# Optimization experiments

Measured on AMD Instinct MI355X. Metric: run time of the kernel, lower is better.

## Reference

```python
import jax, jax.numpy as jnp
import numpy as np

S, B, I = 512, 64, 1024
H = 1024 // 2  # per-direction hidden (MyBiGRU halves hidden_size)


def _gru(x, h0, Wx, Wh, b):
    """Single-direction GRU, faithful to MyGRU.forward.
    x: (S,B,I); h0: (B,H); Wx: (3,I,H) gates [r,u,h]; Wh: (3,H,H); b: (3,H).
    Note: candidate uses (reset_gate * state) @ Whh, matching torch operator
    precedence in `reset_gate * state @ self.weight_hh`.
    """
    # Precompute all input projections once: (S, 3, B, H)
    xg = jnp.einsum('sbi,gih->sgbh', x, Wx)

    def step(h, xt):
        r = jax.nn.sigmoid(xt[0] + h @ Wh[0] + b[0])
        u = jax.nn.sigmoid(xt[1] + h @ Wh[1] + b[1])
        c = jnp.tanh(xt[2] + (r * h) @ Wh[2] + b[2])
        h_new = u * h + (1.0 - u) * c
        return h_new, h_new

    h_last, hs = jax.lax.scan(step, h0, xg)
    return hs, h_last  # (S,B,H), (B,H)


def setup_inputs() -> dict:
    key = jax.random.key(0)
    ks = jax.random.split(key, 6)
    std = jnp.float32(0.01)
    return {
        "x": jax.random.normal(ks[0], (S, B, I), jnp.float32),
        "initial_state": jax.random.normal(ks[1], (B, 2 * H), jnp.float32),
        "Wx_f": std * jax.random.normal(ks[2], (3, I, H), jnp.float32),
        "Wh_f": std * jax.random.normal(ks[3], (3, H, H), jnp.float32),
        "b_f": jnp.zeros((3, H), jnp.float32),
        "Wx_b": std * jax.random.normal(ks[4], (3, I, H), jnp.float32),
        "Wh_b": std * jax.random.normal(ks[5], (3, H, H), jnp.float32),
        "b_b": jnp.zeros((3, H), jnp.float32),
    }


def reference(x, initial_state, Wx_f, Wh_f, b_f, Wx_b, Wh_b, b_b):
    h0_f = initial_state[:, :H]
    h0_b = initial_state[:, H:]
    fwd_out, fwd_state = _gru(x, h0_f, Wx_f, Wh_f, b_f)
    bwd_out, bwd_state = _gru(x[::-1], h0_b, Wx_b, Wh_b, b_b)
    outputs = jnp.concatenate([fwd_out, bwd_out[::-1]], axis=-1)  # (S,B,2H)
    state = jnp.concatenate([fwd_state, bwd_state], axis=-1)      # (B,2H)
    return outputs, state
```

## Files before the change

kernel.cpp:

```cpp
#include <hip/hip_runtime.h>
#include <hip/hip_bf16.h>


typedef __attribute__((ext_vector_type(8))) short short8;
typedef __attribute__((ext_vector_type(4))) float f32x4;

#define SENT 0x7FC0
#define SENT64 0x7FC07FC07FC07FC0ULL

__device__ __forceinline__ unsigned short f2bf(float f) {
    unsigned u = __builtin_bit_cast(unsigned, f);
    u += 0x7FFFu + ((u >> 16) & 1u);
    return (unsigned short)(u >> 16);
}
__device__ __forceinline__ float bf2f(unsigned short h) {
    unsigned u = ((unsigned)h) << 16;
    return __builtin_bit_cast(float, u);
}
__device__ __forceinline__ float xv(unsigned long long p, int jj) {
    return bf2f((unsigned short)(p >> (16 * jj)));
}
__device__ __forceinline__ int imin(int a, int b) { return a < b ? a : b; }


__global__ __launch_bounds__(256) void k_cvt_x(const float* __restrict__ x,
                                               unsigned short* __restrict__ xb) {
    size_t gid = (size_t)blockIdx.x * 256 + threadIdx.x;
    f32x4 a = ((const f32x4*)x)[gid * 2];
    f32x4 b = ((const f32x4*)x)[gid * 2 + 1];
    short8 o;
    o[0] = (short)f2bf(a[0]); o[1] = (short)f2bf(a[1]);
    o[2] = (short)f2bf(a[2]); o[3] = (short)f2bf(a[3]);
    o[4] = (short)f2bf(b[0]); o[5] = (short)f2bf(b[1]);
    o[6] = (short)f2bf(b[2]); o[7] = (short)f2bf(b[3]);
    ((short8*)xb)[gid] = o;
}

__global__ __launch_bounds__(256) void k_cvt_w(const float* __restrict__ Wxf,
                                               const float* __restrict__ Wxb,
                                               unsigned short* __restrict__ wt) {
    int gid = blockIdx.x * 256 + threadIdx.x;
    int n = gid >> 7, kc = gid & 127;
    const float* src = (n < 1536) ? Wxf : Wxb;
    int nn = (n >= 1536) ? n - 1536 : n;
    int g = nn >> 9, h = nn & 511;
    short8 o;
#pragma unroll
    for (int j = 0; j < 8; ++j)
        o[j] = (short)f2bf(src[(size_t)(g * 1024 + kc * 8 + j) * 512 + h]);
    *(short8*)(wt + (size_t)n * 1024 + kc * 8) = o;
}

__global__ __launch_bounds__(256) void k_cvt_whsl(const float* __restrict__ Whf,
                                                  const float* __restrict__ Whb,
                                                  unsigned short* __restrict__ o) {
    int gid = blockIdx.x * 256 + threadIdx.x;
    int kc = gid & 63;
    int r = gid >> 6;
    int c = r & 15; r >>= 4;
    int g = r % 3;  r /= 3;
    int w = r & 31, d = r >> 5;
    const float* src = d ? Whb : Whf;
    short8 v;
#pragma unroll
    for (int j = 0; j < 8; ++j)
        v[j] = (short)f2bf(src[(size_t)(g * 512 + kc * 8 + j) * 512 + w * 16 + c]);
    *(short8*)(o + ((size_t)((d * 32 + w) * 3 + g) * 16 + c) * 512 + kc * 8) = v;
}

__global__ __launch_bounds__(256) void k_sent(unsigned short* __restrict__ h4,
                                              unsigned short* __restrict__ rh4) {
    int gid = blockIdx.x * 256 + threadIdx.x;
    short8 s;
#pragma unroll
    for (int j = 0; j < 8; ++j) s[j] = (short)SENT;
    ((short8*)h4)[gid] = s;
    ((short8*)rh4)[gid] = s;
}

__global__ __launch_bounds__(256) void k_init(const float* __restrict__ h0,
                                              unsigned short* __restrict__ h4) {
    int gid = blockIdx.x * 256 + threadIdx.x;
    int b = gid >> 10, ch = gid & 1023;
    int d = ch >> 9, k = ch & 511;
    h4[((size_t)d * 64 + b) * 512 + k] = f2bf(h0[gid]);
}


__global__ __launch_bounds__(256) void k_gemm(const unsigned short* __restrict__ A,
                                              const unsigned short* __restrict__ Bt,
                                              unsigned short* __restrict__ C) {
    __shared__ unsigned short Al[128 * 40];
    __shared__ unsigned short Bl[128 * 40];
    const int n0 = blockIdx.x * 128;
    const int m0 = blockIdx.y * 128;
    const int t = threadIdx.x, wave = t >> 6, lane = t & 63;
    const int lg = lane >> 4, lr = lane & 15;
    const int wm = wave >> 1, wn = wave & 1;
    const int lrow = t >> 2, lkb = t & 3;

    f32x4 acc[4][4] = {};
    for (int kt = 0; kt < 32; ++kt) {
        const int k0 = kt * 32;
#pragma unroll
        for (int p = 0; p < 2; ++p) {
            int row = lrow + p * 64;
            *(short8*)(Al + row * 40 + lkb * 8) =
                *(const short8*)(A + (size_t)(m0 + row) * 1024 + k0 + lkb * 8);
            *(short8*)(Bl + row * 40 + lkb * 8) =
                *(const short8*)(Bt + (size_t)(n0 + row) * 1024 + k0 + lkb * 8);
        }
        __syncthreads();
        short8 af[4], bfr[4];
#pragma unroll
        for (int mi = 0; mi < 4; ++mi)
            af[mi] = *(const short8*)(Al + (wm * 64 + mi * 16 + lr) * 40 + lg * 8);
#pragma unroll
        for (int ni = 0; ni < 4; ++ni)
            bfr[ni] = *(const short8*)(Bl + (wn * 64 + ni * 16 + lr) * 40 + lg * 8);
#pragma unroll
        for (int mi = 0; mi < 4; ++mi)
#pragma unroll
            for (int ni = 0; ni < 4; ++ni)
                acc[mi][ni] = __builtin_amdgcn_mfma_f32_16x16x32_bf16(af[mi], bfr[ni],
                                                                      acc[mi][ni], 0, 0, 0);
        __syncthreads();
    }
#pragma unroll
    for (int mi = 0; mi < 4; ++mi)
#pragma unroll
        for (int ni = 0; ni < 4; ++ni) {
            int m = m0 + wm * 64 + mi * 16 + lg * 4;
            int n = n0 + wn * 64 + ni * 16 + lr;
            int dd = n >= 1536;
            int nn = n - dd * 1536;
            int g = nn >> 9, h = nn & 511;
            size_t colbase = (size_t)dd * 98304 + (size_t)(h >> 4) * 3072 +
                             (size_t)((h >> 2) & 3) * 12 + g * 4 + (h & 3);
#pragma unroll
            for (int jj = 0; jj < 4; ++jj) {
                int mm = m + jj;
                int s = mm >> 6, brow = mm & 63;
                C[(size_t)s * 196608 + colbase + (size_t)brow * 48] = f2bf(acc[mi][ni][jj]);
            }
        }
}


__device__ __forceinline__ void wait_frag(const char* p, short8* fr) {
    for (;;) {
        asm volatile(
            "global_load_dwordx4 %0, %16, off sc1\n\t"
            "global_load_dwordx4 %1, %16, off offset:64 sc1\n\t"
            "global_load_dwordx4 %2, %16, off offset:128 sc1\n\t"
            "global_load_dwordx4 %3, %16, off offset:192 sc1\n\t"
            "global_load_dwordx4 %4, %16, off offset:256 sc1\n\t"
            "global_load_dwordx4 %5, %16, off offset:320 sc1\n\t"
            "global_load_dwordx4 %6, %16, off offset:384 sc1\n\t"
            "global_load_dwordx4 %7, %16, off offset:448 sc1\n\t"
            "global_load_dwordx4 %8, %16, off offset:512 sc1\n\t"
            "global_load_dwordx4 %9, %16, off offset:576 sc1\n\t"
            "global_load_dwordx4 %10, %16, off offset:640 sc1\n\t"
            "global_load_dwordx4 %11, %16, off offset:704 sc1\n\t"
            "global_load_dwordx4 %12, %16, off offset:768 sc1\n\t"
            "global_load_dwordx4 %13, %16, off offset:832 sc1\n\t"
            "global_load_dwordx4 %14, %16, off offset:896 sc1\n\t"
            "global_load_dwordx4 %15, %16, off offset:960 sc1"
            : "=v"(fr[0]), "=v"(fr[1]), "=v"(fr[2]), "=v"(fr[3]),
              "=v"(fr[4]), "=v"(fr[5]), "=v"(fr[6]), "=v"(fr[7]),
              "=v"(fr[8]), "=v"(fr[9]), "=v"(fr[10]), "=v"(fr[11]),
              "=v"(fr[12]), "=v"(fr[13]), "=v"(fr[14]), "=v"(fr[15])
            : "v"(p) : "memory");
        asm volatile("s_waitcnt vmcnt(0)" ::: "memory");
        int bad = 0;
#pragma unroll
        for (int i = 0; i < 16; ++i)
            bad |= (((unsigned short)fr[i][0]) == SENT) |
                   (((unsigned short)fr[i][4]) == SENT);
        if (!__any(bad)) break;
        __builtin_amdgcn_s_sleep(2);
    }
    __builtin_amdgcn_sched_barrier(0);
}


__global__ __launch_bounds__(320) void k_rec(const unsigned short* __restrict__ xgr,
                                             const unsigned short* __restrict__ whsl,
                                             const float* __restrict__ h0,
                                             const float* __restrict__ b_f,
                                             const float* __restrict__ b_b,
                                             unsigned long long* h4,
                                             unsigned long long* rh4,
                                             float* __restrict__ out) {
    __shared__ char Wlb[98304];
    __shared__ char xls[24576];
    __shared__ int xg_ready;
    __shared__ int xg_ack[4];

    const int w = blockIdx.x;
    const int t = threadIdx.x;
    const int wave5 = t >> 6, lane = t & 63;

    if (t == 0) {
        xg_ready = 0;
        xg_ack[0] = xg_ack[1] = xg_ack[2] = xg_ack[3] = 0;
    }
    for (int i = 0; i < 20; ++i) {
        int c = t + i * 320;
        if (c < 6144) {
            int half = (c >= 3072);
            int byte = (c - half * 3072) << 4;
            int swz = byte ^ (((byte >> 10) & 7) << 4);
            *(short8*)(Wlb + half * 49152 + swz) =
                *(const short8*)((const char*)whsl + (size_t)(half * 32 + w) * 49152 + byte);
        }
    }
    __syncthreads();

    if (wave5 == 4) {
        for (int it = 0; it < 512; ++it) {
            if (it >= 2) {
                for (;;) {
                    int a0 = __hip_atomic_load(&xg_ack[0], __ATOMIC_RELAXED, __HIP_MEMORY_SCOPE_WORKGROUP);
                    int a1 = __hip_atomic_load(&xg_ack[1], __ATOMIC_RELAXED, __HIP_MEMORY_SCOPE_WORKGROUP);
                    int a2 = __hip_atomic_load(&xg_ack[2], __ATOMIC_RELAXED, __HIP_MEMORY_SCOPE_WORKGROUP);
                    int a3 = __hip_atomic_load(&xg_ack[3], __ATOMIC_RELAXED, __HIP_MEMORY_SCOPE_WORKGROUP);
                    if (imin(imin(a0, a1), imin(a2, a3)) >= it - 1) break;
                    __builtin_amdgcn_s_sleep(1);
                }
            }
            const char* pf = (const char*)xgr + (size_t)it * 393216 +
                             (size_t)w * 6144 + lane * 96;
            const char* pb = (const char*)xgr + (size_t)(511 - it) * 393216 + 196608 +
                             (size_t)w * 6144 + lane * 96;
            short8 vf[6], vb[6];
#pragma unroll
            for (int k = 0; k < 6; ++k) {
                vf[k] = *(const short8*)(pf + k * 16);
                vb[k] = *(const short8*)(pb + k * 16);
            }
            char* dst = xls + (it & 1) * 12288 + lane * 96;
#pragma unroll
            for (int k = 0; k < 6; ++k) {
                *(short8*)(dst + k * 16) = vf[k];
                *(short8*)(dst + 6144 + k * 16) = vb[k];
            }
            __builtin_amdgcn_fence(__ATOMIC_RELEASE, "workgroup");
            if (lane == 0)
                __hip_atomic_store(&xg_ready, it + 1, __ATOMIC_RELAXED, __HIP_MEMORY_SCOPE_WORKGROUP);
        }
        return;
    }

    const int wave = wave5, lg = lane >> 4, lr = lane & 15;
    const int b = wave * 16 + lr;
    const int cc = w * 16 + lg * 4;
    const int cswz = (lr & 7) << 4;

    const f32x4 bRf = *(const f32x4*)(b_f + cc);
    const f32x4 bUf = *(const f32x4*)(b_f + 512 + cc);
    const f32x4 bCf = *(const f32x4*)(b_f + 1024 + cc);
    const f32x4 bRb = *(const f32x4*)(b_b + cc);
    const f32x4 bUb = *(const f32x4*)(b_b + 512 + cc);
    const f32x4 bCb = *(const f32x4*)(b_b + 1024 + cc);

    float hf[4], hbo[4];
#pragma unroll
    for (int jj = 0; jj < 4; ++jj) {
        hf[jj]  = h0[(size_t)b * 1024 + cc + jj];
        hbo[jj] = h0[(size_t)b * 1024 + 512 + cc + jj];
    }

    const size_t rof = (size_t)b * 1024;
    const size_t rob = (size_t)(64 + b) * 1024;
    const int fro  = lg * 16;
    const int pubo = w * 32 + lg * 8;
    const int xoff = (b * 4 + lg) * 24;
    char* hbP = (char*)h4;
    char* rbP = (char*)rh4;

    for (int it = 0; it < 512; ++it) {
        const size_t slot  = (size_t)(it & 3) << 17;
        const size_t nslot = (size_t)((it + 1) & 3) << 17;
        const size_t oslot = (size_t)((it + 3) & 3) << 17;

        short8 fr[16];
        wait_frag(hbP + slot + rof + fro, fr);
        __hip_atomic_store((unsigned long long*)(hbP + oslot + rof + pubo), SENT64,
                           __ATOMIC_RELAXED, __HIP_MEMORY_SCOPE_AGENT);

        while (__hip_atomic_load(&xg_ready, __ATOMIC_RELAXED, __HIP_MEMORY_SCOPE_WORKGROUP) < it + 1)
            __builtin_amdgcn_s_sleep(1);
        __builtin_amdgcn_fence(__ATOMIC_ACQUIRE, "workgroup");
        const char* xp = xls + (it & 1) * 12288 + xoff;
        const unsigned long long xfR = *(const unsigned long long*)(xp);
        const unsigned long long xfU = *(const unsigned long long*)(xp + 8);
        const unsigned long long xfC = *(const unsigned long long*)(xp + 16);
        const unsigned long long xbR = *(const unsigned long long*)(xp + 6144);
        const unsigned long long xbU = *(const unsigned long long*)(xp + 6144 + 8);
        const unsigned long long xbC = *(const unsigned long long*)(xp + 6144 + 16);

        f32x4 aR = {0.f, 0.f, 0.f, 0.f}, aU = {0.f, 0.f, 0.f, 0.f};
#pragma unroll
        for (int ks = 0; ks < 16; ++ks) {
            int koff = ks * 64 + lg * 16;
            short8 w0 = *(const short8*)(Wlb + (((lr << 10) + koff) ^ cswz));
            short8 w1 = *(const short8*)(Wlb + ((16384 + (lr << 10) + koff) ^ cswz));
            aR = __builtin_amdgcn_mfma_f32_16x16x32_bf16(w0, fr[ks], aR, 0, 0, 0);
            aU = __builtin_amdgcn_mfma_f32_16x16x32_bf16(w1, fr[ks], aU, 0, 0, 0);
        }
        float uf[4];
        {
            unsigned long long rhp = 0;
#pragma unroll
            for (int jj = 0; jj < 4; ++jj) {
                float pr = aR[jj] + xv(xfR, jj) + bRf[jj];
                float pu = aU[jj] + xv(xfU, jj) + bUf[jj];
                float r = 1.f / (1.f + __expf(-pr));
                uf[jj] = 1.f / (1.f + __expf(-pu));
                rhp |= (unsigned long long)f2bf(r * hf[jj]) << (16 * jj);
            }
            __hip_atomic_store((unsigned long long*)(rbP + slot + rof + pubo), rhp,
                               __ATOMIC_RELAXED, __HIP_MEMORY_SCOPE_AGENT);
        }

        short8 fb[16];
        wait_frag(hbP + slot + rob + fro, fb);
        __hip_atomic_store((unsigned long long*)(hbP + oslot + rob + pubo), SENT64,
                           __ATOMIC_RELAXED, __HIP_MEMORY_SCOPE_AGENT);

        f32x4 cR = {0.f, 0.f, 0.f, 0.f}, cU = {0.f, 0.f, 0.f, 0.f};
#pragma unroll
        for (int ks = 0; ks < 16; ++ks) {
            int koff = ks * 64 + lg * 16;
            short8 w0 = *(const short8*)(Wlb + 49152 + (((lr << 10) + koff) ^ cswz));
            short8 w1 = *(const short8*)(Wlb + 49152 + ((16384 + (lr << 10) + koff) ^ cswz));
            cR = __builtin_amdgcn_mfma_f32_16x16x32_bf16(w0, fb[ks], cR, 0, 0, 0);
            cU = __builtin_amdgcn_mfma_f32_16x16x32_bf16(w1, fb[ks], cU, 0, 0, 0);
        }
        float ub[4];
        {
            unsigned long long rhp = 0;
#pragma unroll
            for (int jj = 0; jj < 4; ++jj) {
                float pr = cR[jj] + xv(xbR, jj) + bRb[jj];
                float pu = cU[jj] + xv(xbU, jj) + bUb[jj];
                float r = 1.f / (1.f + __expf(-pr));
                ub[jj] = 1.f / (1.f + __expf(-pu));
                rhp |= (unsigned long long)f2bf(r * hbo[jj]) << (16 * jj);
            }
            __hip_atomic_store((unsigned long long*)(rbP + slot + rob + pubo), rhp,
                               __ATOMIC_RELAXED, __HIP_MEMORY_SCOPE_AGENT);
        }

        short8 gr[16];
        wait_frag(rbP + slot + rof + fro, gr);
        __hip_atomic_store((unsigned long long*)(rbP + oslot + rof + pubo), SENT64,
                           __ATOMIC_RELAXED, __HIP_MEMORY_SCOPE_AGENT);

        f32x4 aC = {0.f, 0.f, 0.f, 0.f};
#pragma unroll
        for (int ks = 0; ks < 16; ++ks) {
            int koff = ks * 64 + lg * 16;
            short8 w2 = *(const short8*)(Wlb + ((32768 + (lr << 10) + koff) ^ cswz));
            aC = __builtin_amdgcn_mfma_f32_16x16x32_bf16(w2, gr[ks], aC, 0, 0, 0);
        }
        {
            f32x4 ov;
            unsigned long long hp = 0;
#pragma unroll
            for (int jj = 0; jj < 4; ++jj) {
                float pc = aC[jj] + xv(xfC, jj) + bCf[jj];
                float e = __expf(-2.f * pc);
                float c = 2.f / (1.f + e) - 1.f;
                float hn = uf[jj] * hf[jj] + (1.f - uf[jj]) * c;
                hf[jj] = hn;
                ov[jj] = hn;
                hp |= (unsigned long long)f2bf(hn) << (16 * jj);
            }
            __hip_atomic_store((unsigned long long*)(hbP + nslot + rof + pubo), hp,
                               __ATOMIC_RELAXED, __HIP_MEMORY_SCOPE_AGENT);
            *(f32x4*)(out + ((size_t)it * 64 + b) * 1024 + cc) = ov;
        }

        short8 gb[16];
        wait_frag(rbP + slot + rob + fro, gb);
        __hip_atomic_store((unsigned long long*)(rbP + oslot + rob + pubo), SENT64,
                           __ATOMIC_RELAXED, __HIP_MEMORY_SCOPE_AGENT);

        f32x4 cC = {0.f, 0.f, 0.f, 0.f};
#pragma unroll
        for (int ks = 0; ks < 16; ++ks) {
            int koff = ks * 64 + lg * 16;
            short8 w2 = *(const short8*)(Wlb + 49152 + ((32768 + (lr << 10) + koff) ^ cswz));
            cC = __builtin_amdgcn_mfma_f32_16x16x32_bf16(w2, gb[ks], cC, 0, 0, 0);
        }
        {
            f32x4 ov;
            unsigned long long hp = 0;
#pragma unroll
            for (int jj = 0; jj < 4; ++jj) {
                float pc = cC[jj] + xv(xbC, jj) + bCb[jj];
                float e = __expf(-2.f * pc);
                float c = 2.f / (1.f + e) - 1.f;
                float hn = ub[jj] * hbo[jj] + (1.f - ub[jj]) * c;
                hbo[jj] = hn;
                ov[jj] = hn;
                hp |= (unsigned long long)f2bf(hn) << (16 * jj);
            }
            __hip_atomic_store((unsigned long long*)(hbP + nslot + rob + pubo), hp,
                               __ATOMIC_RELAXED, __HIP_MEMORY_SCOPE_AGENT);
            *(f32x4*)(out + ((size_t)(511 - it) * 64 + b) * 1024 + 512 + cc) = ov;
        }

        if (lane == 0)
            __hip_atomic_store(&xg_ack[wave], it + 1, __ATOMIC_RELAXED, __HIP_MEMORY_SCOPE_WORKGROUP);
    }

    {
        f32x4 of = {hf[0], hf[1], hf[2], hf[3]};
        f32x4 ob = {hbo[0], hbo[1], hbo[2], hbo[3]};
        *(f32x4*)(out + (size_t)33554432 + (size_t)b * 1024 + cc) = of;
        *(f32x4*)(out + (size_t)33554432 + (size_t)b * 1024 + 512 + cc) = ob;
    }
}


extern "C" void kernel_launch(void* const* d_in, const int* in_sizes, int n_in,
                              void* d_out, int out_size, void* d_ws, size_t ws_size,
                              hipStream_t stream) {
    const float* x   = (const float*)d_in[0];
    const float* h0  = (const float*)d_in[1];
    const float* Wxf = (const float*)d_in[2];
    const float* Whf = (const float*)d_in[3];
    const float* bf_ = (const float*)d_in[4];
    const float* Wxb = (const float*)d_in[5];
    const float* Whb = (const float*)d_in[6];
    const float* bb_ = (const float*)d_in[7];
    float* out = (float*)d_out;

    char* ws = (char*)d_ws;
    size_t off = 0;
    auto take = [&](size_t bytes) {
        char* p = ws + off;
        off += (bytes + 255) & ~(size_t)255;
        return p;
    };
    unsigned short* xb   = (unsigned short*)take((size_t)33554432 * 2);
    unsigned short* wt   = (unsigned short*)take((size_t)3072 * 1024 * 2);
    unsigned short* xgr  = (unsigned short*)take((size_t)512 * 196608 * 2);
    unsigned short* whsl = (unsigned short*)take((size_t)2 * 32 * 3 * 16 * 512 * 2);
    unsigned long long* h4  = (unsigned long long*)take((size_t)4 * 131072);
    unsigned long long* rh4 = (unsigned long long*)take((size_t)4 * 131072);

    if (off > ws_size) return;

    hipLaunchKernelGGL(k_cvt_x,    dim3(16384),   dim3(256), 0, stream, x, xb);
    hipLaunchKernelGGL(k_cvt_w,    dim3(1536),    dim3(256), 0, stream, Wxf, Wxb, wt);
    hipLaunchKernelGGL(k_cvt_whsl, dim3(768),     dim3(256), 0, stream, Whf, Whb, whsl);
    hipLaunchKernelGGL(k_sent,     dim3(128),     dim3(256), 0, stream,
                       (unsigned short*)h4, (unsigned short*)rh4);
    hipLaunchKernelGGL(k_init,     dim3(256),     dim3(256), 0, stream, h0,
                       (unsigned short*)h4);
    hipLaunchKernelGGL(k_gemm,     dim3(24, 256), dim3(256), 0, stream, xb, wt, xgr);
    hipLaunchKernelGGL(k_rec,      dim3(32),      dim3(320), 0, stream, xgr, whsl, h0,
                       bf_, bb_, h4, rh4, out);
}
```

Before: 4.901 ms.

## Split forward and backward directions across separate waves in recurrent kernel

```diff
diff --git a/kernel.cpp b/kernel.cpp
--- a/kernel.cpp
+++ b/kernel.cpp
@@ -20,7 +20,6 @@
 __device__ __forceinline__ float xv(unsigned long long p, int jj) {
     return bf2f((unsigned short)(p >> (16 * jj)));
 }
-__device__ __forceinline__ int imin(int a, int b) { return a < b ? a : b; }
 
 
 __global__ __launch_bounds__(256) void k_cvt_x(const float* __restrict__ x,
@@ -178,35 +177,33 @@
             bad |= (((unsigned short)fr[i][0]) == SENT) |
                    (((unsigned short)fr[i][4]) == SENT);
         if (!__any(bad)) break;
-        __builtin_amdgcn_s_sleep(2);
+        __builtin_amdgcn_s_sleep(1);
     }
     __builtin_amdgcn_sched_barrier(0);
 }
 
 
-__global__ __launch_bounds__(320) void k_rec(const unsigned short* __restrict__ xgr,
-                                             const unsigned short* __restrict__ whsl,
-                                             const float* __restrict__ h0,
-                                             const float* __restrict__ b_f,
-                                             const float* __restrict__ b_b,
-                                             unsigned long long* h4,
-                                             unsigned long long* rh4,
-                                             float* __restrict__ out) {
+__global__ __launch_bounds__(576, 1) void k_rec(const unsigned short* __restrict__ xgr,
+                                                const unsigned short* __restrict__ whsl,
+                                                const float* __restrict__ h0,
+                                                const float* __restrict__ b_f,
+                                                const float* __restrict__ b_b,
+                                                unsigned long long* h4,
+                                                unsigned long long* rh4,
+                                                float* __restrict__ out) {
     __shared__ char Wlb[98304];
     __shared__ char xls[24576];
     __shared__ int xg_ready;
-    __shared__ int xg_ack[4];
+    __shared__ int xg_ack[8];
 
     const int w = blockIdx.x;
     const int t = threadIdx.x;
-    const int wave5 = t >> 6, lane = t & 63;
-
-    if (t == 0) {
-        xg_ready = 0;
-        xg_ack[0] = xg_ack[1] = xg_ack[2] = xg_ack[3] = 0;
-    }
-    for (int i = 0; i < 20; ++i) {
-        int c = t + i * 320;
+    const int wv = t >> 6, lane = t & 63;
+
+    if (t == 0) xg_ready = 0;
+    if (t < 8) xg_ack[t] = 0;
+    for (int i = 0; i < 11; ++i) {
+        int c = t + i * 576;
         if (c < 6144) {
             int half = (c >= 3072);
             int byte = (c - half * 3072) << 4;
@@ -217,15 +214,18 @@
     }
     __syncthreads();
 
-    if (wave5 == 4) {
+    if (wv == 8) {
         for (int it = 0; it < 512; ++it) {
             if (it >= 2) {
                 for (;;) {
-                    int a0 = __hip_atomic_load(&xg_ack[0], __ATOMIC_RELAXED, __HIP_MEMORY_SCOPE_WORKGROUP);
-                    int a1 = __hip_atomic_load(&xg_ack[1], __ATOMIC_RELAXED, __HIP_MEMORY_SCOPE_WORKGROUP);
-                    int a2 = __hip_atomic_load(&xg_ack[2], __ATOMIC_RELAXED, __HIP_MEMORY_SCOPE_WORKGROUP);
-                    int a3 = __hip_atomic_load(&xg_ack[3], __ATOMIC_RELAXED, __HIP_MEMORY_SCOPE_WORKGROUP);
-                    if (imin(imin(a0, a1), imin(a2, a3)) >= it - 1) break;
+                    int mn = 0x7FFFFFFF;
+#pragma unroll
+                    for (int q = 0; q < 8; ++q) {
+                        int a = __hip_atomic_load(&xg_ack[q], __ATOMIC_RELAXED,
+                                                  __HIP_MEMORY_SCOPE_WORKGROUP);
+                        mn = a < mn ? a : mn;
+                    }
+                    if (mn >= it - 1) break;
                     __builtin_amdgcn_s_sleep(1);
                 }
             }
@@ -247,122 +247,89 @@
             }
             __builtin_amdgcn_fence(__ATOMIC_RELEASE, "workgroup");
             if (lane == 0)
-                __hip_atomic_store(&xg_ready, it + 1, __ATOMIC_RELAXED, __HIP_MEMORY_SCOPE_WORKGROUP);
+                __hip_atomic_store(&xg_ready, it + 1, __ATOMIC_RELAXED,
+                                   __HIP_MEMORY_SCOPE_WORKGROUP);
         }
         return;
     }
 
-    const int wave = wave5, lg = lane >> 4, lr = lane & 15;
-    const int b = wave * 16 + lr;
+    const int dir = wv >> 2;
+    const int lg = lane >> 4, lr = lane & 15;
+    const int b = (wv & 3) * 16 + lr;
     const int cc = w * 16 + lg * 4;
     const int cswz = (lr & 7) << 4;
-
-    const f32x4 bRf = *(const f32x4*)(b_f + cc);
-    const f32x4 bUf = *(const f32x4*)(b_f + 512 + cc);
-    const f32x4 bCf = *(const f32x4*)(b_f + 1024 + cc);
-    const f32x4 bRb = *(const f32x4*)(b_b + cc);
-    const f32x4 bUb = *(const f32x4*)(b_b + 512 + cc);
-    const f32x4 bCb = *(const f32x4*)(b_b + 1024 + cc);
-
-    float hf[4], hbo[4];
-#pragma unroll
-    for (int jj = 0; jj < 4; ++jj) {
-        hf[jj]  = h0[(size_t)b * 1024 + cc + jj];
-        hbo[jj] = h0[(size_t)b * 1024 + 512 + cc + jj];
-    }
-
-    const size_t rof = (size_t)b * 1024;
-    const size_t rob = (size_t)(64 + b) * 1024;
+    const char* Wd = Wlb + dir * 49152;
+    const float* bias = dir ? b_b : b_f;
+
+    const f32x4 bR = *(const f32x4*)(bias + cc);
+    const f32x4 bU = *(const f32x4*)(bias + 512 + cc);
+    const f32x4 bC = *(const f32x4*)(bias + 1024 + cc);
+
+    float hst[4];
+#pragma unroll
+    for (int jj = 0; jj < 4; ++jj)
+        hst[jj] = h0[(size_t)b * 1024 + dir * 512 + cc + jj];
+
+    const size_t row = (size_t)(dir * 64 + b) * 1024;
     const int fro  = lg * 16;
     const int pubo = w * 32 + lg * 8;
-    const int xoff = (b * 4 + lg) * 24;
     char* hbP = (char*)h4;
     char* rbP = (char*)rh4;
 
     for (int it = 0; it < 512; ++it) {
+        const int s = dir ? (511 - it) : it;
         const size_t slot  = (size_t)(it & 3) << 17;
         const size_t nslot = (size_t)((it + 1) & 3) << 17;
         const size_t oslot = (size_t)((it + 3) & 3) << 17;
 
         short8 fr[16];
-        wait_frag(hbP + slot + rof + fro, fr);
-        __hip_atomic_store((unsigned long long*)(hbP + oslot + rof + pubo), SENT64,
+        wait_frag(hbP + slot + row + fro, fr);
+        __hip_atomic_store((unsigned long long*)(hbP + oslot + row + pubo), SENT64,
                            __ATOMIC_RELAXED, __HIP_MEMORY_SCOPE_AGENT);
 
-        while (__hip_atomic_load(&xg_ready, __ATOMIC_RELAXED, __HIP_MEMORY_SCOPE_WORKGROUP) < it + 1)
+        while (__hip_atomic_load(&xg_ready, __ATOMIC_RELAXED,
+                                 __HIP_MEMORY_SCOPE_WORKGROUP) < it + 1)
             __builtin_amdgcn_s_sleep(1);
         __builtin_amdgcn_fence(__ATOMIC_ACQUIRE, "workgroup");
-        const char* xp = xls + (it & 1) * 12288 + xoff;
-        const unsigned long long xfR = *(const unsigned long long*)(xp);
-        const unsigned long long xfU = *(const unsigned long long*)(xp + 8);
-        const unsigned long long xfC = *(const unsigned long long*)(xp + 16);
-        const unsigned long long xbR = *(const unsigned long long*)(xp + 6144);
-        const unsigned long long xbU = *(const unsigned long long*)(xp + 6144 + 8);
-        const unsigned long long xbC = *(const unsigned long long*)(xp + 6144 + 16);
+        const char* xp = xls + (it & 1) * 12288 + dir * 6144 + (b * 4 + lg) * 24;
+        const unsigned long long xR = *(const unsigned long long*)(xp);
+        const unsigned long long xU = *(const unsigned long long*)(xp + 8);
+        const unsigned long long xC = *(const unsigned long long*)(xp + 16);
 
         f32x4 aR = {0.f, 0.f, 0.f, 0.f}, aU = {0.f, 0.f, 0.f, 0.f};
 #pragma unroll
         for (int ks = 0; ks < 16; ++ks) {
             int koff = ks * 64 + lg * 16;
-            short8 w0 = *(const short8*)(Wlb + (((lr << 10) + koff) ^ cswz));
-            short8 w1 = *(const short8*)(Wlb + ((16384 + (lr << 10) + koff) ^ cswz));
+            short8 w0 = *(const short8*)(Wd + (((lr << 10) + koff) ^ cswz));
+            short8 w1 = *(const short8*)(Wd + ((16384 + (lr << 10) + koff) ^ cswz));
             aR = __builtin_amdgcn_mfma_f32_16x16x32_bf16(w0, fr[ks], aR, 0, 0, 0);
             aU = __builtin_amdgcn_mfma_f32_16x16x32_bf16(w1, fr[ks], aU, 0, 0, 0);
         }
-        float uf[4];
+        float uu[4];
         {
             unsigned long long rhp = 0;
 #pragma unroll
             for (int jj = 0; jj < 4; ++jj) {
-                float pr = aR[jj] + xv(xfR, jj) + bRf[jj];
-                float pu = aU[jj] + xv(xfU, jj) + bUf[jj];
+                float pr = aR[jj] + xv(xR, jj) + bR[jj];
+                float pu = aU[jj] + xv(xU, jj) + bU[jj];
                 float r = 1.f / (1.f + __expf(-pr));
-                uf[jj] = 1.f / (1.f + __expf(-pu));
-                rhp |= (unsigned long long)f2bf(r * hf[jj]) << (16 * jj);
-            }
-            __hip_atomic_store((unsigned long long*)(rbP + slot + rof + pubo), rhp,
+                uu[jj] = 1.f / (1.f + __expf(-pu));
+                rhp |= (unsigned long long)f2bf(r * hst[jj]) << (16 * jj);
+            }
+            __hip_atomic_store((unsigned long long*)(rbP + slot + row + pubo), rhp,
                                __ATOMIC_RELAXED, __HIP_MEMORY_SCOPE_AGENT);
         }
 
-        short8 fb[16];
-        wait_frag(hbP + slot + rob + fro, fb);
-        __hip_atomic_store((unsigned long long*)(hbP + oslot + rob + pubo), SENT64,
+        short8 gr[16];
+        wait_frag(rbP + slot + row + fro, gr);
+        __hip_atomic_store((unsigned long long*)(rbP + oslot + row + pubo), SENT64,
                            __ATOMIC_RELAXED, __HIP_MEMORY_SCOPE_AGENT);
 
-        f32x4 cR = {0.f, 0.f, 0.f, 0.f}, cU = {0.f, 0.f, 0.f, 0.f};
+        f32x4 aC = {0.f, 0.f, 0.f, 0.f};
 #pragma unroll
         for (int ks = 0; ks < 16; ++ks) {
             int koff = ks * 64 + lg * 16;
-            short8 w0 = *(const short8*)(Wlb + 49152 + (((lr << 10) + koff) ^ cswz));
-            short8 w1 = *(const short8*)(Wlb + 49152 + ((16384 + (lr << 10) + koff) ^ cswz));
-            cR = __builtin_amdgcn_mfma_f32_16x16x32_bf16(w0, fb[ks], cR, 0, 0, 0);
-            cU = __builtin_amdgcn_mfma_f32_16x16x32_bf16(w1, fb[ks], cU, 0, 0, 0);
-        }
-        float ub[4];
-        {
-            unsigned long long rhp = 0;
-#pragma unroll
-            for (int jj = 0; jj < 4; ++jj) {
-                float pr = cR[jj] + xv(xbR, jj) + bRb[jj];
-                float pu = cU[jj] + xv(xbU, jj) + bUb[jj];
-                float r = 1.f / (1.f + __expf(-pr));
-                ub[jj] = 1.f / (1.f + __expf(-pu));
-                rhp |= (unsigned long long)f2bf(r * hbo[jj]) << (16 * jj);
-            }
-            __hip_atomic_store((unsigned long long*)(rbP + slot + rob + pubo), rhp,
-                               __ATOMIC_RELAXED, __HIP_MEMORY_SCOPE_AGENT);
-        }
-
-        short8 gr[16];
-        wait_frag(rbP + slot + rof + fro, gr);
-        __hip_atomic_store((unsigned long long*)(rbP + oslot + rof + pubo), SENT64,
-                           __ATOMIC_RELAXED, __HIP_MEMORY_SCOPE_AGENT);
-
-        f32x4 aC = {0.f, 0.f, 0.f, 0.f};
-#pragma unroll
-        for (int ks = 0; ks < 16; ++ks) {
-            int koff = ks * 64 + lg * 16;
-            short8 w2 = *(const short8*)(Wlb + ((32768 + (lr << 10) + koff) ^ cswz));
+            short8 w2 = *(const short8*)(Wd + ((32768 + (lr << 10) + koff) ^ cswz));
             aC = __builtin_amdgcn_mfma_f32_16x16x32_bf16(w2, gr[ks], aC, 0, 0, 0);
         }
         {
@@ -370,58 +337,27 @@
             unsigned long long hp = 0;
 #pragma unroll
             for (int jj = 0; jj < 4; ++jj) {
-                float pc = aC[jj] + xv(xfC, jj) + bCf[jj];
+                float pc = aC[jj] + xv(xC, jj) + bC[jj];
                 float e = __expf(-2.f * pc);
                 float c = 2.f / (1.f + e) - 1.f;
-                float hn = uf[jj] * hf[jj] + (1.f - uf[jj]) * c;
-                hf[jj] = hn;
+                float hn = uu[jj] * hst[jj] + (1.f - uu[jj]) * c;
+                hst[jj] = hn;
                 ov[jj] = hn;
                 hp |= (unsigned long long)f2bf(hn) << (16 * jj);
             }
-            __hip_atomic_store((unsigned long long*)(hbP + nslot + rof + pubo), hp,
+            __hip_atomic_store((unsigned long long*)(hbP + nslot + row + pubo), hp,
                                __ATOMIC_RELAXED, __HIP_MEMORY_SCOPE_AGENT);
-            *(f32x4*)(out + ((size_t)it * 64 + b) * 1024 + cc) = ov;
-        }
-
-        short8 gb[16];
-        wait_frag(rbP + slot + rob + fro, gb);
-        __hip_atomic_store((unsigned long long*)(rbP + oslot + rob + pubo), SENT64,
-                           __ATOMIC_RELAXED, __HIP_MEMORY_SCOPE_AGENT);
-
-        f32x4 cC = {0.f, 0.f, 0.f, 0.f};
-#pragma unroll
-        for (int ks = 0; ks < 16; ++ks) {
-            int koff = ks * 64 + lg * 16;
-            short8 w2 = *(const short8*)(Wlb + 49152 + ((32768 + (lr << 10) + koff) ^ cswz));
-            cC = __builtin_amdgcn_mfma_f32_16x16x32_bf16(w2, gb[ks], cC, 0, 0, 0);
-        }
-        {
-            f32x4 ov;
-            unsigned long long hp = 0;
-#pragma unroll
-            for (int jj = 0; jj < 4; ++jj) {
-                float pc = cC[jj] + xv(xbC, jj) + bCb[jj];
-                float e = __expf(-2.f * pc);
-                float c = 2.f / (1.f + e) - 1.f;
-                float hn = ub[jj] * hbo[jj] + (1.f - ub[jj]) * c;
-                hbo[jj] = hn;
-                ov[jj] = hn;
-                hp |= (unsigned long long)f2bf(hn) << (16 * jj);
-            }
-            __hip_atomic_store((unsigned long long*)(hbP + nslot + rob + pubo), hp,
-                               __ATOMIC_RELAXED, __HIP_MEMORY_SCOPE_AGENT);
-            *(f32x4*)(out + ((size_t)(511 - it) * 64 + b) * 1024 + 512 + cc) = ov;
+            *(f32x4*)(out + ((size_t)s * 64 + b) * 1024 + dir * 512 + cc) = ov;
         }
 
         if (lane == 0)
-            __hip_atomic_store(&xg_ack[wave], it + 1, __ATOMIC_RELAXED, __HIP_MEMORY_SCOPE_WORKGROUP);
+            __hip_atomic_store(&xg_ack[wv], it + 1, __ATOMIC_RELAXED,
+                               __HIP_MEMORY_SCOPE_WORKGROUP);
     }
 
     {
-        f32x4 of = {hf[0], hf[1], hf[2], hf[3]};
-        f32x4 ob = {hbo[0], hbo[1], hbo[2], hbo[3]};
-        *(f32x4*)(out + (size_t)33554432 + (size_t)b * 1024 + cc) = of;
-        *(f32x4*)(out + (size_t)33554432 + (size_t)b * 1024 + 512 + cc) = ob;
+        f32x4 of = {hst[0], hst[1], hst[2], hst[3]};
+        *(f32x4*)(out + (size_t)33554432 + (size_t)b * 1024 + dir * 512 + cc) = of;
     }
 }
 
@@ -463,6 +399,6 @@
     hipLaunchKernelGGL(k_init,     dim3(256),     dim3(256), 0, stream, h0,
                        (unsigned short*)h4);
     hipLaunchKernelGGL(k_gemm,     dim3(24, 256), dim3(256), 0, stream, xb, wt, xgr);
-    hipLaunchKernelGGL(k_rec,      dim3(32),      dim3(320), 0, stream, xgr, whsl, h0,
+    hipLaunchKernelGGL(k_rec,      dim3(32),      dim3(576), 0, stream, xgr, whsl, h0,
                        bf_, bb_, h4, rh4, out);
 }
```

After: 9.092 ms. +85.5%, slower.

## Prefetch next recurrent fragments speculatively with partial vmcnt waits

Applied to the files above, without the earlier changes.

```diff
diff --git a/kernel.cpp b/kernel.cpp
--- a/kernel.cpp
+++ b/kernel.cpp
@@ -147,39 +147,59 @@
 }
 
 
+__device__ __forceinline__ void load16(const char* p, short8* fr) {
+    asm volatile(
+        "global_load_dwordx4 %0, %16, off sc1\n\t"
+        "global_load_dwordx4 %1, %16, off offset:64 sc1\n\t"
+        "global_load_dwordx4 %2, %16, off offset:128 sc1\n\t"
+        "global_load_dwordx4 %3, %16, off offset:192 sc1\n\t"
+        "global_load_dwordx4 %4, %16, off offset:256 sc1\n\t"
+        "global_load_dwordx4 %5, %16, off offset:320 sc1\n\t"
+        "global_load_dwordx4 %6, %16, off offset:384 sc1\n\t"
+        "global_load_dwordx4 %7, %16, off offset:448 sc1\n\t"
+        "global_load_dwordx4 %8, %16, off offset:512 sc1\n\t"
+        "global_load_dwordx4 %9, %16, off offset:576 sc1\n\t"
+        "global_load_dwordx4 %10, %16, off offset:640 sc1\n\t"
+        "global_load_dwordx4 %11, %16, off offset:704 sc1\n\t"
+        "global_load_dwordx4 %12, %16, off offset:768 sc1\n\t"
+        "global_load_dwordx4 %13, %16, off offset:832 sc1\n\t"
+        "global_load_dwordx4 %14, %16, off offset:896 sc1\n\t"
+        "global_load_dwordx4 %15, %16, off offset:960 sc1"
+        : "=v"(fr[0]), "=v"(fr[1]), "=v"(fr[2]), "=v"(fr[3]),
+          "=v"(fr[4]), "=v"(fr[5]), "=v"(fr[6]), "=v"(fr[7]),
+          "=v"(fr[8]), "=v"(fr[9]), "=v"(fr[10]), "=v"(fr[11]),
+          "=v"(fr[12]), "=v"(fr[13]), "=v"(fr[14]), "=v"(fr[15])
+        : "v"(p) : "memory");
+}
+
+__device__ __forceinline__ int chk(const short8* fr) {
+    int bad = 0;
+#pragma unroll
+    for (int i = 0; i < 16; ++i)
+        bad |= (((unsigned short)fr[i][0]) == SENT) |
+               (((unsigned short)fr[i][4]) == SENT);
+    return __any(bad);
+}
+
 __device__ __forceinline__ void wait_frag(const char* p, short8* fr) {
     for (;;) {
-        asm volatile(
-            "global_load_dwordx4 %0, %16, off sc1\n\t"
-            "global_load_dwordx4 %1, %16, off offset:64 sc1\n\t"
-            "global_load_dwordx4 %2, %16, off offset:128 sc1\n\t"
-            "global_load_dwordx4 %3, %16, off offset:192 sc1\n\t"
-            "global_load_dwordx4 %4, %16, off offset:256 sc1\n\t"
-            "global_load_dwordx4 %5, %16, off offset:320 sc1\n\t"
-            "global_load_dwordx4 %6, %16, off offset:384 sc1\n\t"
-            "global_load_dwordx4 %7, %16, off offset:448 sc1\n\t"
-            "global_load_dwordx4 %8, %16, off offset:512 sc1\n\t"
-            "global_load_dwordx4 %9, %16, off offset:576 sc1\n\t"
-            "global_load_dwordx4 %10, %16, off offset:640 sc1\n\t"
-            "global_load_dwordx4 %11, %16, off offset:704 sc1\n\t"
-            "global_load_dwordx4 %12, %16, off offset:768 sc1\n\t"
-            "global_load_dwordx4 %13, %16, off offset:832 sc1\n\t"
-            "global_load_dwordx4 %14, %16, off offset:896 sc1\n\t"
-            "global_load_dwordx4 %15, %16, off offset:960 sc1"
-            : "=v"(fr[0]), "=v"(fr[1]), "=v"(fr[2]), "=v"(fr[3]),
-              "=v"(fr[4]), "=v"(fr[5]), "=v"(fr[6]), "=v"(fr[7]),
-              "=v"(fr[8]), "=v"(fr[9]), "=v"(fr[10]), "=v"(fr[11]),
-              "=v"(fr[12]), "=v"(fr[13]), "=v"(fr[14]), "=v"(fr[15])
-            : "v"(p) : "memory");
+        load16(p, fr);
         asm volatile("s_waitcnt vmcnt(0)" ::: "memory");
-        int bad = 0;
-#pragma unroll
-        for (int i = 0; i < 16; ++i)
-            bad |= (((unsigned short)fr[i][0]) == SENT) |
-                   (((unsigned short)fr[i][4]) == SENT);
-        if (!__any(bad)) break;
+        __builtin_amdgcn_sched_barrier(0);
+        if (!chk(fr)) break;
         __builtin_amdgcn_s_sleep(2);
     }
+}
+
+template<int N> __device__ __forceinline__ void wait_vm() {
+    asm volatile("s_waitcnt vmcnt(%0)" :: "i"(N) : "memory");
+}
+
+template<int N>
+__device__ __forceinline__ void check_or_wait(const char* p, short8* fr) {
+    wait_vm<N>();
+    __builtin_amdgcn_sched_barrier(0);
+    if (chk(fr)) wait_frag(p, fr);
     __builtin_amdgcn_sched_barrier(0);
 }
 
@@ -279,13 +299,17 @@
     char* hbP = (char*)h4;
     char* rbP = (char*)rh4;
 
+    short8 fr0[16], fr1[16];
+    load16(hbP + rof + fro, fr0);
+    load16(hbP + rob + fro, fr1);
+
     for (int it = 0; it < 512; ++it) {
         const size_t slot  = (size_t)(it & 3) << 17;
         const size_t nslot = (size_t)((it + 1) & 3) << 17;
         const size_t oslot = (size_t)((it + 3) & 3) << 17;
 
-        short8 fr[16];
-        wait_frag(hbP + slot + rof + fro, fr);
+        if (it == 0) check_or_wait<16>(hbP + slot + rof + fro, fr0);
+        else         check_or_wait<20>(hbP + slot + rof + fro, fr0);
         __hip_atomic_store((unsigned long long*)(hbP + oslot + rof + pubo), SENT64,
                            __ATOMIC_RELAXED, __HIP_MEMORY_SCOPE_AGENT);
 
@@ -306,8 +330,8 @@
             int koff = ks * 64 + lg * 16;
             short8 w0 = *(const short8*)(Wlb + (((lr << 10) + koff) ^ cswz));
             short8 w1 = *(const short8*)(Wlb + ((16384 + (lr << 10) + koff) ^ cswz));
-            aR = __builtin_amdgcn_mfma_f32_16x16x32_bf16(w0, fr[ks], aR, 0, 0, 0);
-            aU = __builtin_amdgcn_mfma_f32_16x16x32_bf16(w1, fr[ks], aU, 0, 0, 0);
+            aR = __builtin_amdgcn_mfma_f32_16x16x32_bf16(w0, fr0[ks], aR, 0, 0, 0);
+            aU = __builtin_amdgcn_mfma_f32_16x16x32_bf16(w1, fr0[ks], aU, 0, 0, 0);
         }
         float uf[4];
         {
@@ -323,9 +347,10 @@
             __hip_atomic_store((unsigned long long*)(rbP + slot + rof + pubo), rhp,
                                __ATOMIC_RELAXED, __HIP_MEMORY_SCOPE_AGENT);
         }
-
-        short8 fb[16];
-        wait_frag(hbP + slot + rob + fro, fb);
+        __builtin_amdgcn_sched_barrier(0);
+        load16(rbP + slot + rof + fro, fr0);
+
+        check_or_wait<18>(hbP + slot + rob + fro, fr1);
         __hip_atomic_store((unsigned long long*)(hbP + oslot + rob + pubo), SENT64,
                            __ATOMIC_RELAXED, __HIP_MEMORY_SCOPE_AGENT);
 
@@ -335,8 +360,8 @@
             int koff = ks * 64 + lg * 16;
             short8 w0 = *(const short8*)(Wlb + 49152 + (((lr << 10) + koff) ^ cswz));
             short8 w1 = *(const short8*)(Wlb + 49152 + ((16384 + (lr << 10) + koff) ^ cswz));
-            cR = __builtin_amdgcn_mfma_f32_16x16x32_bf16(w0, fb[ks], cR, 0, 0, 0);
-            cU = __builtin_amdgcn_mfma_f32_16x16x32_bf16(w1, fb[ks], cU, 0, 0, 0);
+            cR = __builtin_amdgcn_mfma_f32_16x16x32_bf16(w0, fr1[ks], cR, 0, 0, 0);
+            cU = __builtin_amdgcn_mfma_f32_16x16x32_bf16(w1, fr1[ks], cU, 0, 0, 0);
         }
         float ub[4];
         {
@@ -352,9 +377,10 @@
             __hip_atomic_store((unsigned long long*)(rbP + slot + rob + pubo), rhp,
                                __ATOMIC_RELAXED, __HIP_MEMORY_SCOPE_AGENT);
         }
-
-        short8 gr[16];
-        wait_frag(rbP + slot + rof + fro, gr);
+        __builtin_amdgcn_sched_barrier(0);
+        load16(rbP + slot + rob + fro, fr1);
+
+        check_or_wait<18>(rbP + slot + rof + fro, fr0);
         __hip_atomic_store((unsigned long long*)(rbP + oslot + rof + pubo), SENT64,
                            __ATOMIC_RELAXED, __HIP_MEMORY_SCOPE_AGENT);
 
@@ -363,10 +389,10 @@
         for (int ks = 0; ks < 16; ++ks) {
             int koff = ks * 64 + lg * 16;
             short8 w2 = *(const short8*)(Wlb + ((32768 + (lr << 10) + koff) ^ cswz));
-            aC = __builtin_amdgcn_mfma_f32_16x16x32_bf16(w2, gr[ks], aC, 0, 0, 0);
-        }
+            aC = __builtin_amdgcn_mfma_f32_16x16x32_bf16(w2, fr0[ks], aC, 0, 0, 0);
+        }
+        f32x4 ovf;
         {
-            f32x4 ov;
             unsigned long long hp = 0;
 #pragma unroll
             for (int jj = 0; jj < 4; ++jj) {
@@ -375,16 +401,17 @@
                 float c = 2.f / (1.f + e) - 1.f;
                 float hn = uf[jj] * hf[jj] + (1.f - uf[jj]) * c;
                 hf[jj] = hn;
-                ov[jj] = hn;
+                ovf[jj] = hn;
                 hp |= (unsigned long long)f2bf(hn) << (16 * jj);
             }
             __hip_atomic_store((unsigned long long*)(hbP + nslot + rof + pubo), hp,
                                __ATOMIC_RELAXED, __HIP_MEMORY_SCOPE_AGENT);
-            *(f32x4*)(out + ((size_t)it * 64 + b) * 1024 + cc) = ov;
-        }
-
-        short8 gb[16];
-        wait_frag(rbP + slot + rob + fro, gb);
+        }
+        __builtin_amdgcn_sched_barrier(0);
+        load16(hbP + nslot + rof + fro, fr0);
+        *(f32x4*)(out + ((size_t)it * 64 + b) * 1024 + cc) = ovf;
+
+        check_or_wait<19>(rbP + slot + rob + fro, fr1);
         __hip_atomic_store((unsigned long long*)(rbP + oslot + rob + pubo), SENT64,
                            __ATOMIC_RELAXED, __HIP_MEMORY_SCOPE_AGENT);
 
@@ -393,10 +420,10 @@
         for (int ks = 0; ks < 16; ++ks) {
             int koff = ks * 64 + lg * 16;
             short8 w2 = *(const short8*)(Wlb + 49152 + ((32768 + (lr << 10) + koff) ^ cswz));
-            cC = __builtin_amdgcn_mfma_f32_16x16x32_bf16(w2, gb[ks], cC, 0, 0, 0);
-        }
+            cC = __builtin_amdgcn_mfma_f32_16x16x32_bf16(w2, fr1[ks], cC, 0, 0, 0);
+        }
+        f32x4 ovb;
         {
-            f32x4 ov;
             unsigned long long hp = 0;
 #pragma unroll
             for (int jj = 0; jj < 4; ++jj) {
@@ -405,13 +432,15 @@
                 float c = 2.f / (1.f + e) - 1.f;
                 float hn = ub[jj] * hbo[jj] + (1.f - ub[jj]) * c;
                 hbo[jj] = hn;
-                ov[jj] = hn;
+                ovb[jj] = hn;
                 hp |= (unsigned long long)f2bf(hn) << (16 * jj);
             }
             __hip_atomic_store((unsigned long long*)(hbP + nslot + rob + pubo), hp,
                                __ATOMIC_RELAXED, __HIP_MEMORY_SCOPE_AGENT);
-            *(f32x4*)(out + ((size_t)(511 - it) * 64 + b) * 1024 + 512 + cc) = ov;
-        }
+        }
+        __builtin_amdgcn_sched_barrier(0);
+        load16(hbP + nslot + rob + fro, fr1);
+        *(f32x4*)(out + ((size_t)(511 - it) * 64 + b) * 1024 + 512 + cc) = ovb;
 
         if (lane == 0)
             __hip_atomic_store(&xg_ack[wave], it + 1, __ATOMIC_RELAXED, __HIP_MEMORY_SCOPE_WORKGROUP);
```

After: 11.30 ms. 2.31x slower.
